# Optimization experiments

Hardware: AMD Instinct MI355X
Metric: run time of the kernel (lower is better)

## Reference

```python
import jax, jax.numpy as jnp
import numpy as np

B, S, F, H, Dh = 1, 2048, 1024, 16, 64


def rel_shift(x):
    # x: [qlen, klen, B, H] -- Transformer-XL relative shift
    q, k = x.shape[0], x.shape[1]
    x_padded = jnp.pad(x, ((0, 0), (1, 0), (0, 0), (0, 0)))
    x_padded = x_padded.reshape((k + 1, q) + x.shape[2:])
    return x_padded[1:].reshape(x.shape)


def setup_inputs() -> dict:
    key = jax.random.key(0)
    ks = jax.random.split(key, 14)
    sc = 1.0 / np.sqrt(F)
    return {
        "inputs_q": jax.random.normal(ks[0], (B, S, F), jnp.float32),
        "pos_emb": jax.random.normal(ks[1], (S, F), jnp.float32),
        "r_w_bias": jax.random.normal(ks[2], (H, Dh), jnp.float32) * 0.02,
        "r_r_bias": jax.random.normal(ks[3], (H, Dh), jnp.float32) * 0.02,
        "Wq": jax.random.normal(ks[4], (F, H, Dh), jnp.float32) * sc,
        "bq": jnp.zeros((H, Dh), jnp.float32),
        "Wk": jax.random.normal(ks[5], (F, H, Dh), jnp.float32) * sc,
        "bk": jnp.zeros((H, Dh), jnp.float32),
        "Wv": jax.random.normal(ks[6], (F, H, Dh), jnp.float32) * sc,
        "bv": jnp.zeros((H, Dh), jnp.float32),
        "Wr": jax.random.normal(ks[7], (F, H, Dh), jnp.float32) * sc,
        "br": jnp.zeros((H, Dh), jnp.float32),
        "Wo": jax.random.normal(ks[8], (H, Dh, F), jnp.float32) * (1.0 / np.sqrt(H * Dh)),
        "bo": jnp.zeros((F,), jnp.float32),
    }


def reference(inputs_q, pos_emb, r_w_bias, r_r_bias, Wq, bq, Wk, bk, Wv, bv, Wr, br, Wo, bo):
    # QKV projections: [B,S,F] x [F,H,Dh] -> [B,S,H,Dh]
    q = jnp.einsum('bsf,fhd->bshd', inputs_q, Wq) + bq
    k = jnp.einsum('bsf,fhd->bshd', inputs_q, Wk) + bk
    v = jnp.einsum('bsf,fhd->bshd', inputs_q, Wv) + bv
    # relative position key projection: [S,F] -> [S,H,Dh]
    r_key = jnp.einsum('sf,fhd->shd', pos_emb[-k.shape[1]:], Wr) + br
    # content (AC) and position (BD) score terms, layout [i, j, B, H]
    AC = jnp.einsum('bihd,bjhd->ijbh', q + r_w_bias, k)
    BD = jnp.einsum('bihd,jhd->ijbh', q + r_r_bias, r_key)
    BD = rel_shift(BD)
    depth = jnp.asarray(q.shape[-1], jnp.float32)
    attn_score = ((AC + BD) / jnp.sqrt(depth)).transpose((2, 3, 0, 1))  # [B,H,S,S]
    # causal mask -> additive bias (0 where allowed, -1e10 where disallowed)
    seq = q.shape[1]
    causal = jnp.tril(jnp.ones((seq, seq), dtype=bool))[None, None]
    attn_score = attn_score + jnp.where(causal, 0.0, -1e10).astype(attn_score.dtype)
    probs = jax.nn.softmax(attn_score, axis=-1)
    out = jnp.einsum('bhij,bjhd->bihd', probs, v)  # [B,S,H,Dh]
    return jnp.einsum('bihd,hdf->bif', out, Wo) + bo  # [B,S,F]
```

## Files before the change

### kernel.cpp

```cpp
#include <hip/hip_runtime.h>

#define S 2048
#define F 1024
#define H 16
#define DH 64
#define NH (H * DH)

typedef __attribute__((ext_vector_type(8))) short bf16x8;
typedef __attribute__((ext_vector_type(4))) float f32x4;

#define QSCALE 0.1803368801111244f

__device__ __forceinline__ ushort f2bf(float f) {
  unsigned u = __float_as_uint(f);
  u = (u + 0x7FFFu + ((u >> 16) & 1u)) >> 16;
  return (ushort)u;
}
__device__ __forceinline__ float bf2f(ushort u) {
  return __uint_as_float(((unsigned)u) << 16);
}
__device__ __forceinline__ float ex2(float x) {
  float r;
  asm volatile("v_exp_f32 %0, %1\ns_nop 0" : "=v"(r) : "v"(x));
  return r;
}

__device__ __forceinline__ void gload16(const void* g, void* l) {
  __builtin_amdgcn_global_load_lds(
      (const __attribute__((address_space(1))) void*)g,
      (__attribute__((address_space(3))) void*)l, 16, 0, 0);
}

__device__ __forceinline__ bf16x8 ldsT(const ushort* buf, int row, int kbyte) {
  return *(const bf16x8*)((const char*)buf + row * 128 +
                          (kbyte ^ ((row & 7) << 4)));
}

__global__ __launch_bounds__(256) void prep(
    const float* __restrict__ inq, const float* __restrict__ pos,
    const float* __restrict__ Wq, const float* __restrict__ Wk,
    const float* __restrict__ Wv, const float* __restrict__ Wr,
    const float* __restrict__ Wo, ushort* __restrict__ A_bf,
    ushort* __restrict__ P_bf, ushort* __restrict__ Wqkv,
    ushort* __restrict__ Wrt, ushort* __restrict__ Wot) {
  __shared__ ushort T[64][72];
  const int b = blockIdx.x;
  const int t = threadIdx.x;
  if (b < 4096) {
    const float* src = (b < 2048) ? inq : pos;
    ushort* dst = (b < 2048) ? A_bf : P_bf;
    const int i = ((b & 2047) * 256 + t) * 4;
    const float4 v = *(const float4*)(src + i);
    ushort4 u;
    u.x = f2bf(v.x); u.y = f2bf(v.y); u.z = f2bf(v.z); u.w = f2bf(v.w);
    *(ushort4*)(dst + i) = u;
    return;
  }
  const int bb = b - 4096;
  const int which = bb >> 8;
  const int sub = bb & 255;
  const float* src = which == 0 ? Wq
                     : which == 1 ? Wk
                     : which == 2 ? Wv
                     : which == 3 ? Wr : Wo;
  ushort* dst = which == 0 ? Wqkv
                : which == 1 ? Wqkv + 1024 * 1024
                : which == 2 ? Wqkv + 2048 * 1024
                : which == 3 ? Wrt : Wot;
  const int r0 = (sub >> 4) * 64, c0 = (sub & 15) * 64;
#pragma unroll
  for (int q = 0; q < 4; ++q) {
    const int row = q * 16 + (t >> 4);
    const int col = (t & 15) * 4;
    const float4 v = *(const float4*)(src + (size_t)(r0 + row) * 1024 + c0 + col);
    T[row][col + 0] = f2bf(v.x);
    T[row][col + 1] = f2bf(v.y);
    T[row][col + 2] = f2bf(v.z);
    T[row][col + 3] = f2bf(v.w);
  }
  __syncthreads();
#pragma unroll
  for (int q = 0; q < 4; ++q) {
    const int orow = q * 16 + (t >> 4);
    const int ocol = (t & 15) * 4;
    ushort4 u;
    u.x = T[ocol + 0][orow];
    u.y = T[ocol + 1][orow];
    u.z = T[ocol + 2][orow];
    u.w = T[ocol + 3][orow];
    *(ushort4*)(dst + (size_t)(c0 + orow) * 1024 + r0 + ocol) = u;
  }
}

template <int EPI>
__global__ __launch_bounds__(256, 2) void mm128(
    const ushort* __restrict__ A0, const ushort* __restrict__ A1,
    const ushort* __restrict__ B0, const ushort* __restrict__ B1,
    const float* __restrict__ c0, const float* __restrict__ c1,
    const float* __restrict__ c2, const float* __restrict__ c3,
    const float* __restrict__ c4, const float* __restrict__ c5,
    ushort* __restrict__ o0, ushort* __restrict__ o1, ushort* __restrict__ o2,
    ushort* __restrict__ o3, ushort* __restrict__ o4, float* __restrict__ of) {
  __shared__ __align__(16) ushort Asb[2][128 * 64];
  __shared__ __align__(16) ushort Bsb[2][128 * 64];
  const int tid = threadIdx.x;
  const int l = tid & 63, w = tid >> 6;
  const int wm = w >> 1, wn = w & 1;
  const int bz = (EPI == 0) ? blockIdx.z : 0;
  if (EPI == 0 && bz == 1 && blockIdx.x >= 8) return;
  const ushort* Ause = (EPI == 0 && bz) ? A1 : A0;
  const ushort* Buse = (EPI == 0 && bz) ? B1 : B0;
  const int m0 = blockIdx.y * 128, n0 = blockIdx.x * 128;
  const int K = 1024;

  f32x4 acc[4][4];
#pragma unroll
  for (int m = 0; m < 4; ++m)
#pragma unroll
    for (int n = 0; n < 4; ++n) acc[m][n] = (f32x4){0.f, 0.f, 0.f, 0.f};

#define M128_STAGE(c, kt)                                                      \
  {                                                                            \
    const int k0 = (kt) * 64;                                                  \
    _Pragma("unroll") for (int i = 0; i < 4; ++i) {                            \
      const int LB = (i * 256 + tid) * 16, row = LB >> 7, rb_ = LB & 127;      \
      const int tb = rb_ ^ ((row & 7) << 4);                                   \
      gload16((const char*)Ause + ((size_t)(m0 + row) * K + k0) * 2 + tb,      \
              (char*)Asb[c] + LB);                                             \
      gload16((const char*)Buse + ((size_t)(n0 + row) * K + k0) * 2 + tb,      \
              (char*)Bsb[c] + LB);                                             \
    }                                                                          \
  }

  M128_STAGE(0, 0);
  __syncthreads();
  int cur = 0;
#pragma unroll 1
  for (int kt = 0; kt < 16; ++kt) {
    if (kt + 1 < 16) M128_STAGE(cur ^ 1, kt + 1);
#pragma unroll
    for (int ks = 0; ks < 2; ++ks) {
      bf16x8 af[4], bfr[4];
#pragma unroll
      for (int m = 0; m < 4; ++m)
        af[m] = ldsT(Asb[cur], wm * 64 + m * 16 + (l & 15),
                     ks * 64 + (l >> 4) * 16);
#pragma unroll
      for (int n = 0; n < 4; ++n)
        bfr[n] = ldsT(Bsb[cur], wn * 64 + n * 16 + (l & 15),
                      ks * 64 + (l >> 4) * 16);
      __builtin_amdgcn_s_setprio(1);
#pragma unroll
      for (int m = 0; m < 4; ++m)
#pragma unroll
        for (int n = 0; n < 4; ++n)
          acc[m][n] = __builtin_amdgcn_mfma_f32_16x16x32_bf16(
              af[m], bfr[n], acc[m][n], 0, 0, 0);
      __builtin_amdgcn_s_setprio(0);
    }
    __syncthreads();
    cur ^= 1;
  }

#pragma unroll
  for (int m = 0; m < 4; ++m)
#pragma unroll
    for (int n = 0; n < 4; ++n) {
      const int rowb = m0 + wm * 64 + m * 16 + (l >> 4) * 4;
      const int colg = n0 + wn * 64 + n * 16 + (l & 15);
      if constexpr (EPI == 1) {
        const float bs = c0[colg];
#pragma unroll
        for (int r = 0; r < 4; ++r)
          of[(size_t)(rowb + r) * 1024 + colg] = acc[m][n][r] + bs;
      } else if (bz == 1) {
        const float bs = c5[colg];
#pragma unroll
        for (int r = 0; r < 4; ++r)
          o4[(size_t)(rowb + r) * NH + colg] = f2bf(acc[m][n][r] + bs);
      } else {
        const int band = colg >> 10;
        const int colm = colg & 1023;
        if (band == 0) {
          const float bs = c0[colm], vw = c1[colm], vr = c2[colm];
#pragma unroll
          for (int r = 0; r < 4; ++r) {
            const float v = acc[m][n][r] + bs;
            o0[(size_t)(rowb + r) * NH + colm] = f2bf((v + vw) * QSCALE);
            o1[(size_t)(rowb + r) * NH + colm] = f2bf((v + vr) * QSCALE);
          }
        } else if (band == 1) {
          const float bs = c3[colm];
#pragma unroll
          for (int r = 0; r < 4; ++r)
            o2[(size_t)(rowb + r) * NH + colm] = f2bf(acc[m][n][r] + bs);
        } else {
          const float bs = c4[colm];
          ushort4 u;
          u.x = f2bf(acc[m][n][0] + bs);
          u.y = f2bf(acc[m][n][1] + bs);
          u.z = f2bf(acc[m][n][2] + bs);
          u.w = f2bf(acc[m][n][3] + bs);
          *(ushort4*)(o3 + (size_t)colm * S + rowb) = u;
        }
      }
    }
}

__global__ __launch_bounds__(256, 2) void attn_mfma(
    const ushort* __restrict__ qw, const ushort* __restrict__ qr,
    const ushort* __restrict__ kb, const ushort* __restrict__ vt,
    const ushort* __restrict__ rb, float* __restrict__ accA,
    float* __restrict__ accB, float* __restrict__ mA, float* __restrict__ lA,
    float* __restrict__ mB, float* __restrict__ lB) {
  __shared__ __align__(16) ushort Kb[2][64 * 64];
  __shared__ __align__(16) ushort Vb[2][64 * 64];
  __shared__ __align__(16) ushort Rb[2][64 * 64];
  __shared__ __align__(16) ushort BDb[2][64 * 68];
  __shared__ __align__(16) ushort Pb[4][16 * 64];

  const int bx = blockIdx.x;
  const int it = 31 - (bx >> 5);
  const int half = (bx >> 4) & 1;
  const int h = bx & 15;
  const int i0 = it * 64;
  const int tid = threadIdx.x;
  const int l = tid & 63, w = tid >> 6;
  const int lo = (it + 1) >> 1;
  const int fr_base = w * 16 + (l >> 4) * 4;

  float* __restrict__ accX = half ? accB : accA;
  float* __restrict__ mX = half ? mB : mA;
  float* __restrict__ lX = half ? lB : lA;

  if (half == 1 && lo == 0) {
#pragma unroll
    for (int n = 0; n < 4; ++n)
#pragma unroll
      for (int r = 0; r < 4; ++r)
        accX[(size_t)(i0 + fr_base + r) * NH + h * 64 + n * 16 + (l & 15)] =
            0.f;
    if ((l & 15) == 0)
#pragma unroll
      for (int r = 0; r < 4; ++r) {
        mX[(i0 + fr_base + r) * H + h] = -1e30f;
        lX[(i0 + fr_base + r) * H + h] = 0.f;
      }
    return;
  }

  const int jstart = half ? (lo - 1) : it;
  const int jend = half ? 0 : lo;
  const int tp0 = it - jstart;

#pragma unroll
  for (int i = 0; i < 2; ++i) {
    const int LB = (i * 256 + tid) * 16, row = LB >> 7, rb_ = LB & 127;
    gload16((const char*)qw + ((size_t)(i0 + row) * NH + h * 64) * 2 + rb_,
            (char*)Kb[0] + LB);
    gload16((const char*)qr + ((size_t)(i0 + row) * NH + h * 64) * 2 + rb_,
            (char*)Kb[1] + LB);
  }
  __syncthreads();
  bf16x8 qwf[2], qrf[2];
#pragma unroll
  for (int ks = 0; ks < 2; ++ks) {
    const int row = w * 16 + (l & 15);
    const int kbyte = ks * 64 + (l >> 4) * 16;
    qwf[ks] = *(const bf16x8*)((const char*)Kb[0] + row * 128 + kbyte);
    qrf[ks] = *(const bf16x8*)((const char*)Kb[1] + row * 128 + kbyte);
  }
  __syncthreads();

  f32x4 acc_o[4];
#pragma unroll
  for (int n = 0; n < 4; ++n) acc_o[n] = (f32x4){0.f, 0.f, 0.f, 0.f};
  f32x4 acc_l = (f32x4){0.f, 0.f, 0.f, 0.f};
  float m_r[4] = {-1e30f, -1e30f, -1e30f, -1e30f};

  const short one_bf = (short)0x3F80;
  const bf16x8 ones = {one_bf, one_bf, one_bf, one_bf,
                       one_bf, one_bf, one_bf, one_bf};

#define AT_STAGE(c, jt_)                                                       \
  {                                                                            \
    const int j0 = (jt_) * 64;                                                 \
    const int tp_ = it - (jt_);                                                \
    _Pragma("unroll") for (int i = 0; i < 2; ++i) {                            \
      const int LB = (i * 256 + tid) * 16, row = LB >> 7, rb_ = LB & 127;      \
      const int tb = rb_ ^ ((row & 7) << 4);                                   \
      gload16((const char*)kb + ((size_t)(j0 + row) * NH + h * 64) * 2 + tb,   \
              (char*)Kb[c] + LB);                                              \
      gload16((const char*)vt + ((size_t)(h * 64 + row) * S + j0) * 2 + tb,    \
              (char*)Vb[c] + LB);                                              \
      gload16((const char*)rb +                                                \
                  ((size_t)(S - 1 - 64 * tp_ - row) * NH + h * 64) * 2 + tb,   \
              (char*)Rb[c] + LB);                                              \
    }                                                                          \
  }

  if (half) {
#pragma unroll
    for (int i = 0; i < 2; ++i) {
      const int LB = (i * 256 + tid) * 16, row = LB >> 7, rb_ = LB & 127;
      const int tb = rb_ ^ ((row & 7) << 4);
      gload16((const char*)rb +
                  ((size_t)(S - 1 - 64 * (tp0 - 1) - row) * NH + h * 64) * 2 +
                  tb,
              (char*)Rb[1] + LB);
    }
  }
  AT_STAGE(0, jstart);
  __syncthreads();
  if (half) {
    f32x4 bd[4];
#pragma unroll
    for (int n = 0; n < 4; ++n) bd[n] = (f32x4){0.f, 0.f, 0.f, 0.f};
#pragma unroll
    for (int ks = 0; ks < 2; ++ks) {
      bf16x8 rf[4];
#pragma unroll
      for (int n = 0; n < 4; ++n)
        rf[n] = ldsT(Rb[1], n * 16 + (l & 15), ks * 64 + (l >> 4) * 16);
      __builtin_amdgcn_s_setprio(1);
#pragma unroll
      for (int n = 0; n < 4; ++n)
        bd[n] = __builtin_amdgcn_mfma_f32_16x16x32_bf16(qrf[ks], rf[n], bd[n],
                                                        0, 0, 0);
      __builtin_amdgcn_s_setprio(0);
    }
    ushort* B = BDb[(tp0 - 1) & 1];
#pragma unroll
    for (int n = 0; n < 4; ++n)
#pragma unroll
      for (int r = 0; r < 4; ++r)
        B[(fr_base + r) * 68 + n * 16 + (l & 15)] = f2bf(bd[n][r]);
    __syncthreads();
  }

  int cur = 0;
  for (int jt = jstart; jt >= jend; --jt) {
    const int tp = it - jt;
    if (jt > jend) AT_STAGE(cur ^ 1, jt - 1);

    f32x4 bd[4];
#pragma unroll
    for (int n = 0; n < 4; ++n) bd[n] = (f32x4){0.f, 0.f, 0.f, 0.f};
#pragma unroll
    for (int ks = 0; ks < 2; ++ks) {
      bf16x8 rf[4];
#pragma unroll
      for (int n = 0; n < 4; ++n)
        rf[n] = ldsT(Rb[cur], n * 16 + (l & 15), ks * 64 + (l >> 4) * 16);
      __builtin_amdgcn_s_setprio(1);
#pragma unroll
      for (int n = 0; n < 4; ++n)
        bd[n] = __builtin_amdgcn_mfma_f32_16x16x32_bf16(qrf[ks], rf[n], bd[n],
                                                        0, 0, 0);
      __builtin_amdgcn_s_setprio(0);
    }
    {
      ushort* B = BDb[tp & 1];
#pragma unroll
      for (int n = 0; n < 4; ++n)
#pragma unroll
        for (int r = 0; r < 4; ++r)
          B[(fr_base + r) * 68 + n * 16 + (l & 15)] = f2bf(bd[n][r]);
    }

    f32x4 sa[4];
#pragma unroll
    for (int n = 0; n < 4; ++n) sa[n] = (f32x4){0.f, 0.f, 0.f, 0.f};
#pragma unroll
    for (int ks = 0; ks < 2; ++ks) {
      bf16x8 kf[4];
#pragma unroll
      for (int n = 0; n < 4; ++n)
        kf[n] = ldsT(Kb[cur], n * 16 + (l & 15), ks * 64 + (l >> 4) * 16);
      __builtin_amdgcn_s_setprio(1);
#pragma unroll
      for (int n = 0; n < 4; ++n)
        sa[n] = __builtin_amdgcn_mfma_f32_16x16x32_bf16(qwf[ks], kf[n], sa[n],
                                                        0, 0, 0);
      __builtin_amdgcn_s_setprio(0);
    }

    const ushort* Bnew = BDb[tp & 1];
    const ushort* Bold = BDb[(tp & 1) ^ 1];
    float p[4][4];
    float rmax[4] = {-1e30f, -1e30f, -1e30f, -1e30f};
#pragma unroll
    for (int n = 0; n < 4; ++n)
#pragma unroll
      for (int r = 0; r < 4; ++r) {
        const int fr = fr_base + r;
        const int jj = n * 16 + (l & 15);
        const int u = 64 + fr - jj;
        const float bdv =
            bf2f((u >= 64) ? Bnew[fr * 68 + (u - 64)] : Bold[fr * 68 + u]);
        float s = sa[n][r] + bdv;
        if (tp == 0 && jj > fr) s = -1e30f;
        p[n][r] = s;
        rmax[r] = fmaxf(rmax[r], s);
      }
#pragma unroll
    for (int off = 1; off < 16; off <<= 1)
#pragma unroll
      for (int r = 0; r < 4; ++r)
        rmax[r] = fmaxf(rmax[r], __shfl_xor(rmax[r], off, 64));
    int grow = 0;
#pragma unroll
    for (int r = 0; r < 4; ++r) grow |= (rmax[r] > m_r[r] + 8.f);
    if (__any(grow)) {
      float corr[4];
#pragma unroll
      for (int r = 0; r < 4; ++r) {
        const float mn = fmaxf(m_r[r], rmax[r]);
        corr[r] = ex2(m_r[r] - mn);
        m_r[r] = mn;
      }
#pragma unroll
      for (int r = 0; r < 4; ++r) acc_l[r] *= corr[r];
#pragma unroll
      for (int n = 0; n < 4; ++n)
#pragma unroll
        for (int r = 0; r < 4; ++r) acc_o[n][r] *= corr[r];
    }
#pragma unroll
    for (int n = 0; n < 4; ++n)
#pragma unroll
      for (int r = 0; r < 4; ++r) p[n][r] = ex2(p[n][r] - m_r[r]);

    {
      ushort* P = Pb[w];
#pragma unroll
      for (int n = 0; n < 4; ++n)
#pragma unroll
        for (int r = 0; r < 4; ++r) {
          const int row = (l >> 4) * 4 + r;
          const int colb = (n * 16 + (l & 15)) * 2;
          *(ushort*)((char*)P + row * 128 + (colb ^ ((row & 7) << 4))) =
              f2bf(p[n][r]);
        }
    }

#pragma unroll
    for (int ks = 0; ks < 2; ++ks) {
      const int prow = l & 15;
      const bf16x8 pf = *(const bf16x8*)(
          (const char*)Pb[w] + prow * 128 +
          ((ks * 64 + (l >> 4) * 16) ^ ((prow & 7) << 4)));
      bf16x8 vf[4];
#pragma unroll
      for (int n = 0; n < 4; ++n)
        vf[n] = ldsT(Vb[cur], n * 16 + (l & 15), ks * 64 + (l >> 4) * 16);
      __builtin_amdgcn_s_setprio(1);
#pragma unroll
      for (int n = 0; n < 4; ++n)
        acc_o[n] = __builtin_amdgcn_mfma_f32_16x16x32_bf16(pf, vf[n], acc_o[n],
                                                           0, 0, 0);
      acc_l = __builtin_amdgcn_mfma_f32_16x16x32_bf16(pf, ones, acc_l, 0, 0, 0);
      __builtin_amdgcn_s_setprio(0);
    }
    __syncthreads();
    cur ^= 1;
  }

#pragma unroll
  for (int n = 0; n < 4; ++n)
#pragma unroll
    for (int r = 0; r < 4; ++r)
      accX[(size_t)(i0 + fr_base + r) * NH + h * 64 + n * 16 + (l & 15)] =
          acc_o[n][r];
  if ((l & 15) == 0)
#pragma unroll
    for (int r = 0; r < 4; ++r) {
      mX[(i0 + fr_base + r) * H + h] = m_r[r];
      lX[(i0 + fr_base + r) * H + h] = acc_l[r];
    }
}

__global__ __launch_bounds__(256) void combine_halves(
    const float* __restrict__ accA, const float* __restrict__ accB,
    const float* __restrict__ mA, const float* __restrict__ lA,
    const float* __restrict__ mB, const float* __restrict__ lB,
    ushort* __restrict__ ab) {
  const int idx = blockIdx.x * 256 + threadIdx.x;
  const int base = idx * 4;
  const int i = base >> 10;
  const int h = (base & 1023) >> 6;
  const float4 a = *(const float4*)(accA + base);
  const float4 b = *(const float4*)(accB + base);
  const float ma = mA[i * H + h], la = lA[i * H + h];
  const float mb = mB[i * H + h], lb = lB[i * H + h];
  const float M = fmaxf(ma, mb);
  const float ea = ex2(ma - M), eb = ex2(mb - M);
  const float inv = 1.f / (la * ea + lb * eb);
  ushort4 u;
  u.x = f2bf((a.x * ea + b.x * eb) * inv);
  u.y = f2bf((a.y * ea + b.y * eb) * inv);
  u.z = f2bf((a.z * ea + b.z * eb) * inv);
  u.w = f2bf((a.w * ea + b.w * eb) * inv);
  *(ushort4*)(ab + base) = u;
}

extern "C" void kernel_launch(void* const* d_in, const int* in_sizes, int n_in,
                              void* d_out, int out_size, void* d_ws,
                              size_t ws_size, hipStream_t stream) {
  const float* inq = (const float*)d_in[0];
  const float* pos = (const float*)d_in[1];
  const float* rwb = (const float*)d_in[2];
  const float* rrb = (const float*)d_in[3];
  const float* Wq = (const float*)d_in[4];
  const float* bq = (const float*)d_in[5];
  const float* Wk = (const float*)d_in[6];
  const float* bk = (const float*)d_in[7];
  const float* Wv = (const float*)d_in[8];
  const float* bv = (const float*)d_in[9];
  const float* Wr = (const float*)d_in[10];
  const float* br = (const float*)d_in[11];
  const float* Wo = (const float*)d_in[12];
  const float* bo = (const float*)d_in[13];

  char* ws = (char*)d_ws;
  const size_t MB = 1024 * 1024;
  ushort* A_bf = (ushort*)(ws + 0 * MB);
  ushort* P_bf = (ushort*)(ws + 4 * MB);
  ushort* Wqkv = (ushort*)(ws + 8 * MB);
  ushort* Wrt = (ushort*)(ws + 14 * MB);
  ushort* Wot = (ushort*)(ws + 16 * MB);
  ushort* qwp = (ushort*)(ws + 18 * MB);
  ushort* qrp = (ushort*)(ws + 22 * MB);
  ushort* kbp = (ushort*)(ws + 26 * MB);
  ushort* vtp = (ushort*)(ws + 30 * MB);
  ushort* rbp = (ushort*)(ws + 34 * MB);
  float* mlA = (float*)(ws + 4 * MB);
  float* mA = mlA + 0 * 32768;
  float* lA = mlA + 1 * 32768;
  float* mB = mlA + 2 * 32768;
  float* lB = mlA + 3 * 32768;
  float* accA = (float*)(ws + 6 * MB);
  float* accB = (float*)(ws + 38 * MB);
  ushort* abp = A_bf;

  prep<<<5376, 256, 0, stream>>>(inq, pos, Wq, Wk, Wv, Wr, Wo, A_bf, P_bf,
                                 Wqkv, Wrt, Wot);

  mm128<0><<<dim3(24, 16, 2), 256, 0, stream>>>(
      A_bf, P_bf, Wqkv, Wrt, bq, rwb, rrb, bk, bv, br, qwp, qrp, kbp, vtp, rbp,
      nullptr);

  attn_mfma<<<1024, 256, 0, stream>>>(qwp, qrp, kbp, vtp, rbp, accA, accB, mA,
                                      lA, mB, lB);
  combine_halves<<<2048, 256, 0, stream>>>(accA, accB, mA, lA, mB, lB, abp);

  mm128<1><<<dim3(8, 16, 1), 256, 0, stream>>>(
      abp, nullptr, Wot, nullptr, bo, nullptr, nullptr, nullptr, nullptr,
      nullptr, nullptr, nullptr, nullptr, nullptr, nullptr, (float*)d_out);
}
```

Baseline: 216.5 us.

## Single-buffer K/V in attention to raise occupancy, swizzle GEMM block order

The attention kernel drops double buffering for K and V, removes the separate P buffer by reusing the stale BD half, and raises launch bounds from 2 to 3 blocks per CU, trading prefetch overlap for occupancy. K/V loads now go straight into the single buffer at the start of each iteration, with an extra barrier before use. The GEMM kernel remaps block indices with an 8-way swizzle so neighbouring blocks share tiles in cache. The inline-asm exp2 is replaced by the builtin. Risks: losing the K/V prefetch exposes load latency, and reusing the BD buffer for P needs careful synchronisation.

```diff
diff --git a/kernel.cpp b/kernel.cpp
--- a/kernel.cpp
+++ b/kernel.cpp
@@ -18,11 +18,6 @@
 }
 __device__ __forceinline__ float bf2f(ushort u) {
   return __uint_as_float(((unsigned)u) << 16);
-}
-__device__ __forceinline__ float ex2(float x) {
-  float r;
-  asm volatile("v_exp_f32 %0, %1\ns_nop 0" : "=v"(r) : "v"(x));
-  return r;
 }
 
 __device__ __forceinline__ void gload16(const void* g, void* l) {
@@ -106,11 +101,18 @@
   const int tid = threadIdx.x;
   const int l = tid & 63, w = tid >> 6;
   const int wm = w >> 1, wn = w & 1;
+  constexpr int GX = (EPI == 0) ? 24 : 8;
+  constexpr int GY = 16;
+  constexpr int CPX = GX * GY / 8;
+  const int lin = blockIdx.x + GX * blockIdx.y;
+  const int swz = (lin & 7) * CPX + (lin >> 3);
+  const int bx2 = swz % GX;
+  const int by2 = swz / GX;
   const int bz = (EPI == 0) ? blockIdx.z : 0;
-  if (EPI == 0 && bz == 1 && blockIdx.x >= 8) return;
+  if (EPI == 0 && bz == 1 && bx2 >= 8) return;
   const ushort* Ause = (EPI == 0 && bz) ? A1 : A0;
   const ushort* Buse = (EPI == 0 && bz) ? B1 : B0;
-  const int m0 = blockIdx.y * 128, n0 = blockIdx.x * 128;
+  const int m0 = by2 * 128, n0 = bx2 * 128;
   const int K = 1024;
 
   f32x4 acc[4][4];
@@ -207,17 +209,16 @@
     }
 }
 
-__global__ __launch_bounds__(256, 2) void attn_mfma(
+__global__ __launch_bounds__(256, 3) void attn_mfma(
     const ushort* __restrict__ qw, const ushort* __restrict__ qr,
     const ushort* __restrict__ kb, const ushort* __restrict__ vt,
     const ushort* __restrict__ rb, float* __restrict__ accA,
     float* __restrict__ accB, float* __restrict__ mA, float* __restrict__ lA,
     float* __restrict__ mB, float* __restrict__ lB) {
-  __shared__ __align__(16) ushort Kb[2][64 * 64];
-  __shared__ __align__(16) ushort Vb[2][64 * 64];
+  __shared__ __align__(16) ushort Kb[64 * 64];
+  __shared__ __align__(16) ushort Vb[64 * 64];
   __shared__ __align__(16) ushort Rb[2][64 * 64];
   __shared__ __align__(16) ushort BDb[2][64 * 68];
-  __shared__ __align__(16) ushort Pb[4][16 * 64];
 
   const int bx = blockIdx.x;
   const int it = 31 - (bx >> 5);
@@ -256,62 +257,29 @@
 #pragma unroll
   for (int i = 0; i < 2; ++i) {
     const int LB = (i * 256 + tid) * 16, row = LB >> 7, rb_ = LB & 127;
+    const int tb = rb_ ^ ((row & 7) << 4);
     gload16((const char*)qw + ((size_t)(i0 + row) * NH + h * 64) * 2 + rb_,
-            (char*)Kb[0] + LB);
+            (char*)Kb + LB);
     gload16((const char*)qr + ((size_t)(i0 + row) * NH + h * 64) * 2 + rb_,
-            (char*)Kb[1] + LB);
-  }
-  __syncthreads();
-  bf16x8 qwf[2], qrf[2];
-#pragma unroll
-  for (int ks = 0; ks < 2; ++ks) {
-    const int row = w * 16 + (l & 15);
-    const int kbyte = ks * 64 + (l >> 4) * 16;
-    qwf[ks] = *(const bf16x8*)((const char*)Kb[0] + row * 128 + kbyte);
-    qrf[ks] = *(const bf16x8*)((const char*)Kb[1] + row * 128 + kbyte);
-  }
-  __syncthreads();
-
-  f32x4 acc_o[4];
-#pragma unroll
-  for (int n = 0; n < 4; ++n) acc_o[n] = (f32x4){0.f, 0.f, 0.f, 0.f};
-  f32x4 acc_l = (f32x4){0.f, 0.f, 0.f, 0.f};
-  float m_r[4] = {-1e30f, -1e30f, -1e30f, -1e30f};
-
-  const short one_bf = (short)0x3F80;
-  const bf16x8 ones = {one_bf, one_bf, one_bf, one_bf,
-                       one_bf, one_bf, one_bf, one_bf};
-
-#define AT_STAGE(c, jt_)                                                       \
-  {                                                                            \
-    const int j0 = (jt_) * 64;                                                 \
-    const int tp_ = it - (jt_);                                                \
-    _Pragma("unroll") for (int i = 0; i < 2; ++i) {                            \
-      const int LB = (i * 256 + tid) * 16, row = LB >> 7, rb_ = LB & 127;      \
-      const int tb = rb_ ^ ((row & 7) << 4);                                   \
-      gload16((const char*)kb + ((size_t)(j0 + row) * NH + h * 64) * 2 + tb,   \
-              (char*)Kb[c] + LB);                                              \
-      gload16((const char*)vt + ((size_t)(h * 64 + row) * S + j0) * 2 + tb,    \
-              (char*)Vb[c] + LB);                                              \
-      gload16((const char*)rb +                                                \
-                  ((size_t)(S - 1 - 64 * tp_ - row) * NH + h * 64) * 2 + tb,   \
-              (char*)Rb[c] + LB);                                              \
-    }                                                                          \
-  }
-
-  if (half) {
-#pragma unroll
-    for (int i = 0; i < 2; ++i) {
-      const int LB = (i * 256 + tid) * 16, row = LB >> 7, rb_ = LB & 127;
-      const int tb = rb_ ^ ((row & 7) << 4);
+            (char*)Vb + LB);
+    gload16((const char*)rb +
+                ((size_t)(S - 1 - 64 * tp0 - row) * NH + h * 64) * 2 + tb,
+            (char*)Rb[0] + LB);
+    if (half)
       gload16((const char*)rb +
                   ((size_t)(S - 1 - 64 * (tp0 - 1) - row) * NH + h * 64) * 2 +
                   tb,
               (char*)Rb[1] + LB);
-    }
-  }
-  AT_STAGE(0, jstart);
+  }
   __syncthreads();
+  bf16x8 qwf[2], qrf[2];
+#pragma unroll
+  for (int ks = 0; ks < 2; ++ks) {
+    const int row = w * 16 + (l & 15);
+    const int kbyte = ks * 64 + (l >> 4) * 16;
+    qwf[ks] = *(const bf16x8*)((const char*)Kb + row * 128 + kbyte);
+    qrf[ks] = *(const bf16x8*)((const char*)Vb + row * 128 + kbyte);
+  }
   if (half) {
     f32x4 bd[4];
 #pragma unroll
@@ -329,19 +297,45 @@
                                                         0, 0, 0);
       __builtin_amdgcn_s_setprio(0);
     }
-    ushort* B = BDb[(tp0 - 1) & 1];
+    char* B = (char*)BDb + ((tp0 - 1) & 1) * 8704;
 #pragma unroll
     for (int n = 0; n < 4; ++n)
 #pragma unroll
       for (int r = 0; r < 4; ++r)
-        B[(fr_base + r) * 68 + n * 16 + (l & 15)] = f2bf(bd[n][r]);
-    __syncthreads();
-  }
+        *(ushort*)(B + (fr_base + r) * 136 + (n * 16 + (l & 15)) * 2) =
+            f2bf(bd[n][r]);
+  }
+  __syncthreads();
+
+  f32x4 acc_o[4];
+#pragma unroll
+  for (int n = 0; n < 4; ++n) acc_o[n] = (f32x4){0.f, 0.f, 0.f, 0.f};
+  f32x4 acc_l = (f32x4){0.f, 0.f, 0.f, 0.f};
+  float m_r[4] = {-1e30f, -1e30f, -1e30f, -1e30f};
+
+  const short one_bf = (short)0x3F80;
+  const bf16x8 ones = {one_bf, one_bf, one_bf, one_bf,
+                       one_bf, one_bf, one_bf, one_bf};
 
   int cur = 0;
   for (int jt = jstart; jt >= jend; --jt) {
     const int tp = it - jt;
-    if (jt > jend) AT_STAGE(cur ^ 1, jt - 1);
+    const int j0 = jt * 64;
+
+#pragma unroll
+    for (int i = 0; i < 2; ++i) {
+      const int LB = (i * 256 + tid) * 16, row = LB >> 7, rb_ = LB & 127;
+      const int tb = rb_ ^ ((row & 7) << 4);
+      gload16((const char*)kb + ((size_t)(j0 + row) * NH + h * 64) * 2 + tb,
+              (char*)Kb + LB);
+      gload16((const char*)vt + ((size_t)(h * 64 + row) * S + j0) * 2 + tb,
+              (char*)Vb + LB);
+      if (jt > jend)
+        gload16((const char*)rb +
+                    ((size_t)(S - 1 - 64 * (tp + 1) - row) * NH + h * 64) * 2 +
+                    tb,
+                (char*)Rb[cur ^ 1] + LB);
+    }
 
     f32x4 bd[4];
 #pragma unroll
@@ -360,13 +354,16 @@
       __builtin_amdgcn_s_setprio(0);
     }
     {
-      ushort* B = BDb[tp & 1];
+      char* B = (char*)BDb + (tp & 1) * 8704;
 #pragma unroll
       for (int n = 0; n < 4; ++n)
 #pragma unroll
         for (int r = 0; r < 4; ++r)
-          B[(fr_base + r) * 68 + n * 16 + (l & 15)] = f2bf(bd[n][r]);
-    }
+          *(ushort*)(B + (fr_base + r) * 136 + (n * 16 + (l & 15)) * 2) =
+              f2bf(bd[n][r]);
+    }
+
+    __syncthreads();
 
     f32x4 sa[4];
 #pragma unroll
@@ -376,7 +373,7 @@
       bf16x8 kf[4];
 #pragma unroll
       for (int n = 0; n < 4; ++n)
-        kf[n] = ldsT(Kb[cur], n * 16 + (l & 15), ks * 64 + (l >> 4) * 16);
+        kf[n] = ldsT(Kb, n * 16 + (l & 15), ks * 64 + (l >> 4) * 16);
       __builtin_amdgcn_s_setprio(1);
 #pragma unroll
       for (int n = 0; n < 4; ++n)
@@ -385,8 +382,8 @@
       __builtin_amdgcn_s_setprio(0);
     }
 
-    const ushort* Bnew = BDb[tp & 1];
-    const ushort* Bold = BDb[(tp & 1) ^ 1];
+    const char* Bnew = (const char*)BDb + (tp & 1) * 8704;
+    const char* Bold = (const char*)BDb + ((tp & 1) ^ 1) * 8704;
     float p[4][4];
     float rmax[4] = {-1e30f, -1e30f, -1e30f, -1e30f};
 #pragma unroll
@@ -396,8 +393,9 @@
         const int fr = fr_base + r;
         const int jj = n * 16 + (l & 15);
         const int u = 64 + fr - jj;
-        const float bdv =
-            bf2f((u >= 64) ? Bnew[fr * 68 + (u - 64)] : Bold[fr * 68 + u]);
+        const float bdv = bf2f(*(const ushort*)(
+            (u >= 64) ? Bnew + fr * 136 + (u - 64) * 2
+                      : Bold + fr * 136 + u * 2));
         float s = sa[n][r] + bdv;
         if (tp == 0 && jj > fr) s = -1e30f;
         p[n][r] = s;
@@ -416,7 +414,7 @@
 #pragma unroll
       for (int r = 0; r < 4; ++r) {
         const float mn = fmaxf(m_r[r], rmax[r]);
-        corr[r] = ex2(m_r[r] - mn);
+        corr[r] = __builtin_exp2f(m_r[r] - mn);
         m_r[r] = mn;
       }
 #pragma unroll
@@ -429,18 +427,18 @@
 #pragma unroll
     for (int n = 0; n < 4; ++n)
 #pragma unroll
-      for (int r = 0; r < 4; ++r) p[n][r] = ex2(p[n][r] - m_r[r]);
+      for (int r = 0; r < 4; ++r) p[n][r] = __builtin_exp2f(p[n][r] - m_r[r]);
 
     {
-      ushort* P = Pb[w];
+      char* P = (char*)BDb + ((tp & 1) ^ 1) * 8704;
 #pragma unroll
       for (int n = 0; n < 4; ++n)
 #pragma unroll
         for (int r = 0; r < 4; ++r) {
-          const int row = (l >> 4) * 4 + r;
+          const int row16 = (l >> 4) * 4 + r;
           const int colb = (n * 16 + (l & 15)) * 2;
-          *(ushort*)((char*)P + row * 128 + (colb ^ ((row & 7) << 4))) =
-              f2bf(p[n][r]);
+          *(ushort*)(P + (w * 16 + row16) * 136 +
+                     (colb ^ ((row16 & 7) << 4))) = f2bf(p[n][r]);
         }
     }
 
@@ -448,12 +446,12 @@
     for (int ks = 0; ks < 2; ++ks) {
       const int prow = l & 15;
       const bf16x8 pf = *(const bf16x8*)(
-          (const char*)Pb[w] + prow * 128 +
+          (const char*)BDb + ((tp & 1) ^ 1) * 8704 + (w * 16 + prow) * 136 +
           ((ks * 64 + (l >> 4) * 16) ^ ((prow & 7) << 4)));
       bf16x8 vf[4];
 #pragma unroll
       for (int n = 0; n < 4; ++n)
-        vf[n] = ldsT(Vb[cur], n * 16 + (l & 15), ks * 64 + (l >> 4) * 16);
+        vf[n] = ldsT(Vb, n * 16 + (l & 15), ks * 64 + (l >> 4) * 16);
       __builtin_amdgcn_s_setprio(1);
 #pragma unroll
       for (int n = 0; n < 4; ++n)
@@ -494,7 +492,7 @@
   const float ma = mA[i * H + h], la = lA[i * H + h];
   const float mb = mB[i * H + h], lb = lB[i * H + h];
   const float M = fmaxf(ma, mb);
-  const float ea = ex2(ma - M), eb = ex2(mb - M);
+  const float ea = __builtin_exp2f(ma - M), eb = __builtin_exp2f(mb - M);
   const float inv = 1.f / (la * ea + lb * eb);
   ushort4 u;
   u.x = f2bf((a.x * ea + b.x * eb) * inv);
```

Result: faster. 194.4 us (-10.2%).
